# Kernel optimization log

Hardware: AMD Instinct MI355X
Metric: run time of the kernel (lower is better)

The kernel has to match this reference:

```python
import jax, jax.numpy as jnp
import numpy as np

D_MODEL = 2048
NUM_HEADS = 16
D_K = D_MODEL // NUM_HEADS


def setup_inputs() -> dict:
    key = jax.random.key(0)
    ks = jax.random.split(key, 12)
    B, S, D = 2, 2048, D_MODEL
    s = 1.0 / np.sqrt(D)
    return {
        "q": jax.random.normal(ks[0], (B, S, D), jnp.float32),
        "k": jax.random.normal(ks[1], (B, S, D), jnp.float32),
        "v": jax.random.normal(ks[2], (B, S, D), jnp.float32),
        "Wq": jax.random.normal(ks[3], (D, D), jnp.float32) * s,
        "bq": jax.random.normal(ks[4], (D,), jnp.float32) * 0.01,
        "Wk": jax.random.normal(ks[5], (D, D), jnp.float32) * s,
        "bk": jax.random.normal(ks[6], (D,), jnp.float32) * 0.01,
        "Wv": jax.random.normal(ks[7], (D, D), jnp.float32) * s,
        "bv": jax.random.normal(ks[8], (D,), jnp.float32) * 0.01,
        "Wo": jax.random.normal(ks[9], (D, D), jnp.float32) * s,
        "bo": jax.random.normal(ks[10], (D,), jnp.float32) * 0.01,
    }


def reference(q, k, v, Wq, bq, Wk, bk, Wv, bv, Wo, bo):
    B, S, D = q.shape
    H, dk = NUM_HEADS, D_K

    def proj(x, W, b):
        # Linear then split heads -> [B, H, S, dk]
        y = jnp.einsum('bsd,df->bsf', x, W) + b
        return y.reshape(B, -1, H, dk).transpose(0, 2, 1, 3)

    Q = proj(q, Wq, bq)
    K = proj(k, Wk, bk)
    V = proj(v, Wv, bv)

    scores = jnp.einsum('bhqd,bhkd->bhqk', Q, K) / jnp.sqrt(jnp.float32(dk))
    attn = jax.nn.softmax(scores, axis=-1)  # dropout is identity (eval)
    out = jnp.einsum('bhqk,bhkd->bhqd', attn, V)
    out = out.transpose(0, 2, 1, 3).reshape(B, -1, D)
    return jnp.einsum('bsd,df->bsf', out, Wo) + bo
```

## Files before the change

kernel.cpp:

```cpp
#include <hip/hip_runtime.h>
#include <hip/hip_bf16.h>
#include <stdint.h>

typedef float  f32x4  __attribute__((ext_vector_type(4)));
typedef float  f32x16 __attribute__((ext_vector_type(16)));
typedef short  s16x8  __attribute__((ext_vector_type(8)));

#define D_MODEL 2048
#define NHEADS  16
#define DK      128
#define BATCH   2
#define SEQ     2048
#define MROWS   (BATCH*SEQ)

__device__ __forceinline__ unsigned short f2bf(float f) {
  union { float f; unsigned int u; } v; v.f = f;
  unsigned int r = v.u + 0x7FFFu + ((v.u >> 16) & 1u);
  return (unsigned short)(r >> 16);
}

__device__ __forceinline__ unsigned int packbf_c(float lo, float hi) {
  __hip_bfloat16 l = __float2bfloat16(lo);
  __hip_bfloat16 h = __float2bfloat16(hi);
  unsigned short lu, hu;
  __builtin_memcpy(&lu, &l, 2);
  __builtin_memcpy(&hu, &h, 2);
  return (unsigned int)lu | ((unsigned int)hu << 16);
}

__device__ __forceinline__ void async16(const void* g, void* l) {
  __builtin_amdgcn_global_load_lds(
      (const __attribute__((address_space(1))) unsigned int*)g,
      (__attribute__((address_space(3))) unsigned int*)l,
      16, 0, 0);
}

__global__ __launch_bounds__(256) void f2b3_kernel(const float* __restrict__ q,
                                                   const float* __restrict__ k,
                                                   const float* __restrict__ v,
                                                   unsigned short* __restrict__ qb,
                                                   unsigned short* __restrict__ kb,
                                                   unsigned short* __restrict__ vb) {
  const float* s; unsigned short* d;
  switch (blockIdx.y) {
    case 0:  s = q; d = qb; break;
    case 1:  s = k; d = kb; break;
    default: s = v; d = vb; break;
  }
  int i = blockIdx.x * 256 + threadIdx.x;
  const float4* s4 = (const float4*)s;
  float4 a = s4[2*i];
  float4 b = s4[2*i+1];
  s16x8 o;
  o[0] = (short)f2bf(a.x); o[1] = (short)f2bf(a.y);
  o[2] = (short)f2bf(a.z); o[3] = (short)f2bf(a.w);
  o[4] = (short)f2bf(b.x); o[5] = (short)f2bf(b.y);
  o[6] = (short)f2bf(b.z); o[7] = (short)f2bf(b.w);
  *(s16x8*)(d + 8*(size_t)i) = o;
}

__global__ __launch_bounds__(256) void wtrans_kernel(const float* __restrict__ Wq,
                                                     const float* __restrict__ Wk,
                                                     const float* __restrict__ Wv,
                                                     const float* __restrict__ Wo,
                                                     unsigned short* __restrict__ WqT,
                                                     unsigned short* __restrict__ WkT,
                                                     unsigned short* __restrict__ WvT,
                                                     unsigned short* __restrict__ WoT) {
  const float* W; unsigned short* Wt;
  switch (blockIdx.z) {
    case 0:  W = Wq; Wt = WqT; break;
    case 1:  W = Wk; Wt = WkT; break;
    case 2:  W = Wv; Wt = WvT; break;
    default: W = Wo; Wt = WoT; break;
  }
  __shared__ float tl[32][33];
  int x = threadIdx.x, y = threadIdx.y;
  int n0 = blockIdx.x * 32, k0 = blockIdx.y * 32;
  #pragma unroll
  for (int j = 0; j < 32; j += 8)
    tl[y + j][x] = W[(size_t)(k0 + y + j) * D_MODEL + n0 + x];
  __syncthreads();
  #pragma unroll
  for (int j = 0; j < 32; j += 8)
    Wt[(size_t)(n0 + y + j) * D_MODEL + k0 + x] = f2bf(tl[x][y + j]);
}

__device__ __forceinline__ void gemm3b_core(const unsigned short* __restrict__ A,
                                            const unsigned short* __restrict__ Bt,
                                            const float* __restrict__ bias,
                                            void* __restrict__ Cout,
                                            int N, int K, int mode, float scale,
                                            int m0, int n0, char* lds) {
  const int t  = threadIdx.x;
  const int l  = t & 63, w = t >> 6;
  const int wm = w >> 1, wn = w & 1;
  const int lr = l & 15, lg = l >> 4;

  auto STAGE = [&](int slot, int kt) {
    char* Ad = lds + slot*49152;
    char* Bd = lds + slot*49152 + 32768;
    #pragma unroll
    for (int i = 0; i < 4; ++i) {
      int c = t + 512*i;
      int row = c >> 3, crs = (c & 7) ^ (row & 7);
      async16(A + (size_t)(m0 + row)*K + kt*64 + crs*8, Ad + c*16);
    }
    #pragma unroll
    for (int i = 0; i < 2; ++i) {
      int c = t + 512*i;
      int row = c >> 3, crs = (c & 7) ^ (row & 7);
      async16(Bt + (size_t)(n0 + row)*K + kt*64 + crs*8, Bd + c*16);
    }
  };

  const int NT = K >> 6;
  STAGE(0, 0);
  STAGE(1, 1);
  asm volatile("s_waitcnt vmcnt(6)" ::: "memory");
  __builtin_amdgcn_s_barrier();

  f32x4 acc[4][4] = {};

  for (int kt = 0; kt < NT; ++kt) {
    if (kt + 2 < NT) STAGE((kt + 2) % 3, kt + 2);
    const char* Ac = lds + (kt % 3)*49152;
    const char* Bc = lds + (kt % 3)*49152 + 32768;

    #pragma unroll
    for (int ks = 0; ks < 2; ++ks) {
      const int cb = ks*64 + lg*16;
      s16x8 af[4], bf[4];
      #pragma unroll
      for (int mf = 0; mf < 4; ++mf) {
        int row = wm*64 + mf*16 + lr;
        af[mf] = *(const s16x8*)(Ac + row*128 + (cb ^ ((row & 7) << 4)));
      }
      #pragma unroll
      for (int nf = 0; nf < 4; ++nf) {
        int row = wn*64 + nf*16 + lr;
        bf[nf] = *(const s16x8*)(Bc + row*128 + (cb ^ ((row & 7) << 4)));
      }
      __builtin_amdgcn_s_setprio(1);
      #pragma unroll
      for (int mf = 0; mf < 4; ++mf)
        #pragma unroll
        for (int nf = 0; nf < 4; ++nf)
          acc[mf][nf] = __builtin_amdgcn_mfma_f32_16x16x32_bf16(af[mf], bf[nf], acc[mf][nf], 0, 0, 0);
      __builtin_amdgcn_s_setprio(0);
    }

    if (kt + 1 < NT) {
      if (kt + 2 < NT) asm volatile("s_waitcnt vmcnt(6)" ::: "memory");
      else             asm volatile("s_waitcnt vmcnt(0)" ::: "memory");
      __builtin_amdgcn_s_barrier();
    }
  }

  if (mode == 0) {
    float* C = (float*)Cout;
    #pragma unroll
    for (int nf = 0; nf < 4; ++nf) {
      int col = n0 + wn*64 + nf*16 + lr;
      float bv = bias[col];
      #pragma unroll
      for (int mf = 0; mf < 4; ++mf) {
        int rowb = m0 + wm*64 + mf*16 + lg*4;
        #pragma unroll
        for (int r = 0; r < 4; ++r)
          C[(size_t)(rowb + r)*N + col] = (acc[mf][nf][r] + bv) * scale;
      }
    }
  } else {
    unsigned short* C = (unsigned short*)Cout;
    #pragma unroll
    for (int nf = 0; nf < 4; ++nf) {
      int col = n0 + wn*64 + nf*16 + lr;
      float bv = bias[col];
      int h = col >> 7, dkk = col & 127;
      #pragma unroll
      for (int mf = 0; mf < 4; ++mf) {
        int rowb = m0 + wm*64 + mf*16 + lg*4;
        #pragma unroll
        for (int r = 0; r < 4; ++r) {
          int row = rowb + r;
          int b = row >> 11, s = row & 2047;
          C[((size_t)((b*NHEADS + h)*SEQ + s))*DK + dkk] = f2bf((acc[mf][nf][r] + bv) * scale);
        }
      }
    }
  }
}

__device__ __forceinline__ void swz_mn(int& m0, int& n0) {
  int lin = blockIdx.y * 16 + blockIdx.x;
  int xcd = lin & 7;
  int pos = lin >> 3;
  n0 = (xcd*2 + (pos & 1)) * 128;
  m0 = (pos >> 1) * 256;
}

__global__ __launch_bounds__(512) void gemm256_qkv(const unsigned short* __restrict__ qb,
                                                   const unsigned short* __restrict__ kb,
                                                   const unsigned short* __restrict__ vb,
                                                   const unsigned short* __restrict__ WT,
                                                   const float* __restrict__ bq,
                                                   const float* __restrict__ bk,
                                                   const float* __restrict__ bv,
                                                   unsigned short* __restrict__ Hout,
                                                   float qscale) {
  __shared__ char lds[147456];
  const int z = blockIdx.z;
  const unsigned short* A = (z == 0) ? qb : (z == 1) ? kb : vb;
  const float* bias       = (z == 0) ? bq : (z == 1) ? bk : bv;
  const float scale       = (z == 0) ? qscale : 1.0f;
  const unsigned short* Bt = WT + (size_t)z * D_MODEL * D_MODEL;
  unsigned short* Cout     = Hout + (size_t)z * MROWS * D_MODEL;
  int m0, n0; swz_mn(m0, n0);
  gemm3b_core(A, Bt, bias, Cout, D_MODEL, D_MODEL, 1, scale, m0, n0, lds);
}

__global__ __launch_bounds__(512) void gemm256_out(const unsigned short* __restrict__ A,
                                                   const unsigned short* __restrict__ Bt,
                                                   const float* __restrict__ bias,
                                                   float* __restrict__ Cout) {
  __shared__ char lds[147456];
  int m0, n0; swz_mn(m0, n0);
  gemm3b_core(A, Bt, bias, Cout, D_MODEL, D_MODEL, 0, 1.0f, m0, n0, lds);
}

__global__ __launch_bounds__(256, 2) void attn_kernel(const unsigned short* __restrict__ Q,
                                                      const unsigned short* __restrict__ K,
                                                      const unsigned short* __restrict__ V,
                                                      unsigned short* __restrict__ O) {
  __shared__ char lds[64*256 + 128*144];
  unsigned short* Kl = (unsigned short*)lds;
  unsigned short* Vt = (unsigned short*)(lds + 64*256);

  const int t  = threadIdx.x;
  const int l  = t & 63, w = t >> 6;
  const int q_ = l & 31, hi = l >> 5;
  const int bh = blockIdx.y;
  const int b  = bh >> 4, h = bh & 15;
  const int q0 = blockIdx.x * 128;

  const unsigned short* Qp = Q + (size_t)bh * SEQ * DK;
  const unsigned short* Kp = K + (size_t)bh * SEQ * DK;
  const unsigned short* Vp = V + (size_t)bh * SEQ * DK;

  const int qrow = q0 + w*32 + q_;
  s16x8 aq[8];
  #pragma unroll
  for (int kk = 0; kk < 8; ++kk)
    aq[kk] = *(const s16x8*)(Qp + (size_t)qrow*DK + kk*16 + hi*8);

  f32x16 accO[4] = {};
  float m = -INFINITY, L = 0.f;

  const int vp_ = t & 31;
  const int vd0 = (t >> 5) * 8;

  const int NT = SEQ/64;
  s16x8 va0, vb0, va1, vb1;

  va0 = *(const s16x8*)(Vp + (size_t)(2*vp_    )*DK + vd0);
  vb0 = *(const s16x8*)(Vp + (size_t)(2*vp_ + 1)*DK + vd0);
  va1 = *(const s16x8*)(Vp + (size_t)(2*vp_    )*DK + vd0 + 64);
  vb1 = *(const s16x8*)(Vp + (size_t)(2*vp_ + 1)*DK + vd0 + 64);
  #pragma unroll
  for (int i = 0; i < 4; ++i) {
    int c   = t + 256*i;
    int row = c >> 4;
    int sb  = ((c & 15) << 4) ^ ((row & 15) << 4);
    async16((const char*)(Kp + (size_t)row*DK) + sb, (char*)Kl + c*16);
  }
  asm volatile("" ::: "memory");

  for (int tt = 0; tt < NT; ++tt) {
    asm volatile("s_waitcnt vmcnt(4)" ::: "memory");
    #pragma unroll
    for (int j = 0; j < 8; ++j) {
      unsigned int pk0 = (unsigned int)(unsigned short)va0[j]
                       | ((unsigned int)(unsigned short)vb0[j] << 16);
      *(unsigned int*)&Vt[(vd0 + j)*72 + 2*vp_] = pk0;
      unsigned int pk1 = (unsigned int)(unsigned short)va1[j]
                       | ((unsigned int)(unsigned short)vb1[j] << 16);
      *(unsigned int*)&Vt[(vd0 + 64 + j)*72 + 2*vp_] = pk1;
    }
    __syncthreads();

    f32x16 S0 = {}, S1 = {};
    __builtin_amdgcn_s_setprio(1);
    #pragma unroll
    for (int t2 = 0; t2 < 2; ++t2) {
      int krow = t2*32 + q_;
      const char* kb = (const char*)Kl + krow*256;
      int swz = (krow & 15) << 4;
      #pragma unroll
      for (int kk = 0; kk < 8; ++kk) {
        s16x8 kf = *(const s16x8*)(kb + ((kk*32 + hi*16) ^ swz));
        if (t2 == 0) S0 = __builtin_amdgcn_mfma_f32_32x32x16_bf16(kf, aq[kk], S0, 0, 0, 0);
        else         S1 = __builtin_amdgcn_mfma_f32_32x32x16_bf16(kf, aq[kk], S1, 0, 0, 0);
      }
    }
    __builtin_amdgcn_s_setprio(0);
    __syncthreads();

    if (tt + 1 < NT) {
      int kvn = (tt + 1) * 64;
      va0 = *(const s16x8*)(Vp + (size_t)(kvn + 2*vp_    )*DK + vd0);
      vb0 = *(const s16x8*)(Vp + (size_t)(kvn + 2*vp_ + 1)*DK + vd0);
      va1 = *(const s16x8*)(Vp + (size_t)(kvn + 2*vp_    )*DK + vd0 + 64);
      vb1 = *(const s16x8*)(Vp + (size_t)(kvn + 2*vp_ + 1)*DK + vd0 + 64);
      #pragma unroll
      for (int i = 0; i < 4; ++i) {
        int c   = t + 256*i;
        int row = c >> 4;
        int sb  = ((c & 15) << 4) ^ ((row & 15) << 4);
        async16((const char*)(Kp + (size_t)(kvn + row)*DK) + sb, (char*)Kl + c*16);
      }
      asm volatile("" ::: "memory");
    }

    f32x16 mx;
    #pragma unroll
    for (int r = 0; r < 16; ++r) mx[r] = fmaxf(S0[r], S1[r]);
    float m8_[8];
    #pragma unroll
    for (int r = 0; r < 8; ++r) m8_[r] = fmaxf(mx[r], mx[r+8]);
    float m4a = fmaxf(m8_[0], m8_[4]), m4b = fmaxf(m8_[1], m8_[5]);
    float m4c = fmaxf(m8_[2], m8_[6]), m4d = fmaxf(m8_[3], m8_[7]);
    float pmax = fmaxf(fmaxf(m4a, m4b), fmaxf(m4c, m4d));
    pmax = fmaxf(pmax, __shfl_xor(pmax, 32, 64));

    if (!__all(pmax <= m + 11.0f)) {
      float mnew = fmaxf(m, pmax);
      float corr = exp2f(m - mnew);
      m = mnew;
      L *= corr;
      #pragma unroll
      for (int sub = 0; sub < 4; ++sub)
        #pragma unroll
        for (int r = 0; r < 16; ++r) accO[sub][r] *= corr;
    }

    float rs0 = 0.f, rs1 = 0.f, rs2 = 0.f, rs3 = 0.f;
    #pragma unroll
    for (int r = 0; r < 4; ++r) {
      float a0 = exp2f(S0[r]    - m); S0[r]    = a0; rs0 += a0;
      float a1 = exp2f(S0[r+4]  - m); S0[r+4]  = a1; rs1 += a1;
      float a2 = exp2f(S0[r+8]  - m); S0[r+8]  = a2; rs2 += a2;
      float a3 = exp2f(S0[r+12] - m); S0[r+12] = a3; rs3 += a3;
      float b0 = exp2f(S1[r]    - m); S1[r]    = b0; rs0 += b0;
      float b1 = exp2f(S1[r+4]  - m); S1[r+4]  = b1; rs1 += b1;
      float b2 = exp2f(S1[r+8]  - m); S1[r+8]  = b2; rs2 += b2;
      float b3 = exp2f(S1[r+12] - m); S1[r+12] = b3; rs3 += b3;
    }
    float rs = (rs0 + rs1) + (rs2 + rs3);
    rs += __shfl_xor(rs, 32, 64);
    L += rs;

    s16x8 PB[4];
    #pragma unroll
    for (int t2 = 0; t2 < 2; ++t2) {
      #pragma unroll
      for (int half = 0; half < 2; ++half) {
        int bse = half*8;
        unsigned int pkA01, pkA23, pkB01, pkB23;
        if (t2 == 0) {
          pkA01 = packbf_c(S0[bse+0], S0[bse+1]);
          pkA23 = packbf_c(S0[bse+2], S0[bse+3]);
          pkB01 = packbf_c(S0[bse+4], S0[bse+5]);
          pkB23 = packbf_c(S0[bse+6], S0[bse+7]);
        } else {
          pkA01 = packbf_c(S1[bse+0], S1[bse+1]);
          pkA23 = packbf_c(S1[bse+2], S1[bse+3]);
          pkB01 = packbf_c(S1[bse+4], S1[bse+5]);
          pkB23 = packbf_c(S1[bse+6], S1[bse+7]);
        }
        unsigned int xA01 = __shfl_xor(pkA01, 32, 64);
        unsigned int xA23 = __shfl_xor(pkA23, 32, 64);
        unsigned int xB01 = __shfl_xor(pkB01, 32, 64);
        unsigned int xB23 = __shfl_xor(pkB23, 32, 64);
        union { unsigned int u[4]; s16x8 v; } f;
        f.u[0] = hi ? xB01 : pkA01;
        f.u[1] = hi ? xB23 : pkA23;
        f.u[2] = hi ? pkB01 : xA01;
        f.u[3] = hi ? pkB23 : xA23;
        PB[t2*2 + half] = f.v;
      }
    }

    __builtin_amdgcn_s_setprio(1);
    #pragma unroll
    for (int sub = 0; sub < 4; ++sub) {
      const char* vb2 = (const char*)Vt + (size_t)(sub*32 + q_)*144 + hi*16;
      #pragma unroll
      for (int kk = 0; kk < 4; ++kk) {
        s16x8 vf = *(const s16x8*)(vb2 + kk*32);
        accO[sub] = __builtin_amdgcn_mfma_f32_32x32x16_bf16(vf, PB[kk], accO[sub], 0, 0, 0);
      }
    }
    __builtin_amdgcn_s_setprio(0);

    __builtin_amdgcn_s_barrier();
  }

  __syncthreads();
  unsigned short* Ob = (unsigned short*)lds + (size_t)w*4096;
  float inv = 1.0f / L;
  #pragma unroll
  for (int sub = 0; sub < 4; ++sub)
    #pragma unroll
    for (int j = 0; j < 8; ++j) {
      unsigned int pw = packbf_c(accO[sub][2*j]*inv, accO[sub][2*j+1]*inv);
      int dv = sub*32 + (j&1)*2 + ((j>>1)*8) + 4*hi;
      *(unsigned int*)((char*)Ob + q_*256 + ((dv*2) ^ ((q_ & 15) << 4))) = pw;
    }
  asm volatile("s_waitcnt lgkmcnt(0)" ::: "memory");
  size_t gbase = ((size_t)(b*SEQ + q0 + w*32 + q_))*D_MODEL + h*DK;
  #pragma unroll
  for (int p = 0; p < 8; ++p) {
    int chunk = hi + 2*p;
    s16x8 ov = *(const s16x8*)((char*)Ob + q_*256 + ((chunk*16) ^ ((q_ & 15) << 4)));
    *(s16x8*)(O + gbase + chunk*8) = ov;
  }
}

extern "C" void kernel_launch(void* const* d_in, const int* in_sizes, int n_in,
                              void* d_out, int out_size, void* d_ws, size_t ws_size,
                              hipStream_t stream) {
  const float* q  = (const float*)d_in[0];
  const float* k  = (const float*)d_in[1];
  const float* v  = (const float*)d_in[2];
  const float* Wq = (const float*)d_in[3];
  const float* bq = (const float*)d_in[4];
  const float* Wk = (const float*)d_in[5];
  const float* bk = (const float*)d_in[6];
  const float* Wv = (const float*)d_in[7];
  const float* bv = (const float*)d_in[8];
  const float* Wo = (const float*)d_in[9];
  const float* bo = (const float*)d_in[10];
  float* out = (float*)d_out;

  char* ws = (char*)d_ws;
  const size_t SZT = (size_t)MROWS * D_MODEL * 2;
  const size_t SZW = (size_t)D_MODEL * D_MODEL * 2;

  unsigned short* qb  = (unsigned short*)(ws);
  unsigned short* kb  = (unsigned short*)(ws + SZT);
  unsigned short* vb  = (unsigned short*)(ws + 2*SZT);
  unsigned short* WqT = (unsigned short*)(ws + 3*SZT);
  unsigned short* WkT = (unsigned short*)(ws + 3*SZT + SZW);
  unsigned short* WvT = (unsigned short*)(ws + 3*SZT + 2*SZW);
  unsigned short* WoT = (unsigned short*)(ws + 3*SZT + 3*SZW);
  unsigned short* Qh  = (unsigned short*)(ws + 3*SZT + 4*SZW);
  unsigned short* Kh  = (unsigned short*)(ws + 4*SZT + 4*SZW);
  unsigned short* Vh  = (unsigned short*)(ws + 5*SZT + 4*SZW);
  unsigned short* Oc  = qb;

  const int n8 = MROWS * D_MODEL / 8;
  f2b3_kernel<<<dim3(n8/256, 3), 256, 0, stream>>>(q, k, v, qb, kb, vb);
  wtrans_kernel<<<dim3(64, 64, 4), dim3(32, 8), 0, stream>>>(Wq, Wk, Wv, Wo, WqT, WkT, WvT, WoT);

  const float qscale = 0.1275174308f;
  gemm256_qkv<<<dim3(16, 16, 3), 512, 0, stream>>>(qb, kb, vb, WqT, bq, bk, bv, Qh, qscale);

  attn_kernel<<<dim3(SEQ/128, BATCH*NHEADS), 256, 0, stream>>>(Qh, Kh, Vh, Oc);

  gemm256_out<<<dim3(16, 16), 512, 0, stream>>>(Oc, WoT, bo, out);
}
```

Measured before the change: 309.2 us.

## Emit V transposed from QKV GEMM and async-stage it into double-buffered LDS

The QKV projection GEMM gets a third epilogue mode that writes V in a [b,h,dk,seq] layout. The attention kernel can then stream V tiles straight into LDS with async copies, using an XOR swizzle and two buffers. This removes the per-tile register load, pack and transpose of V into LDS, and the trailing barrier at the end of each iteration. In exchange, the V GEMM epilogue now writes with a large stride and poorer coalescing. Correctness also relies on the loop-top __syncthreads waiting for the async V and K copies, since the explicit vmcnt wait was removed.

```diff
diff --git a/kernel.cpp b/kernel.cpp
--- a/kernel.cpp
+++ b/kernel.cpp
@@ -171,7 +171,7 @@
           C[(size_t)(rowb + r)*N + col] = (acc[mf][nf][r] + bv) * scale;
       }
     }
-  } else {
+  } else if (mode == 1) {
     unsigned short* C = (unsigned short*)Cout;
     #pragma unroll
     for (int nf = 0; nf < 4; ++nf) {
@@ -186,6 +186,24 @@
           int row = rowb + r;
           int b = row >> 11, s = row & 2047;
           C[((size_t)((b*NHEADS + h)*SEQ + s))*DK + dkk] = f2bf((acc[mf][nf][r] + bv) * scale);
+        }
+      }
+    }
+  } else {
+    unsigned short* C = (unsigned short*)Cout;
+    #pragma unroll
+    for (int nf = 0; nf < 4; ++nf) {
+      int col = n0 + wn*64 + nf*16 + lr;
+      float bv = bias[col];
+      int h = col >> 7, dkk = col & 127;
+      #pragma unroll
+      for (int mf = 0; mf < 4; ++mf) {
+        int rowb = m0 + wm*64 + mf*16 + lg*4;
+        #pragma unroll
+        for (int r = 0; r < 4; ++r) {
+          int row = rowb + r;
+          int b = row >> 11, s = row & 2047;
+          C[((size_t)((b*NHEADS + h)*DK + dkk))*SEQ + s] = f2bf((acc[mf][nf][r] + bv) * scale);
         }
       }
     }
@@ -214,10 +232,11 @@
   const unsigned short* A = (z == 0) ? qb : (z == 1) ? kb : vb;
   const float* bias       = (z == 0) ? bq : (z == 1) ? bk : bv;
   const float scale       = (z == 0) ? qscale : 1.0f;
+  const int   mode        = (z == 2) ? 2 : 1;
   const unsigned short* Bt = WT + (size_t)z * D_MODEL * D_MODEL;
   unsigned short* Cout     = Hout + (size_t)z * MROWS * D_MODEL;
   int m0, n0; swz_mn(m0, n0);
-  gemm3b_core(A, Bt, bias, Cout, D_MODEL, D_MODEL, 1, scale, m0, n0, lds);
+  gemm3b_core(A, Bt, bias, Cout, D_MODEL, D_MODEL, mode, scale, m0, n0, lds);
 }
 
 __global__ __launch_bounds__(512) void gemm256_out(const unsigned short* __restrict__ A,
@@ -231,11 +250,10 @@
 
 __global__ __launch_bounds__(256, 2) void attn_kernel(const unsigned short* __restrict__ Q,
                                                       const unsigned short* __restrict__ K,
-                                                      const unsigned short* __restrict__ V,
+                                                      const unsigned short* __restrict__ Vt_g,
                                                       unsigned short* __restrict__ O) {
-  __shared__ char lds[64*256 + 128*144];
+  __shared__ char lds[64*256 + 2*16384];
   unsigned short* Kl = (unsigned short*)lds;
-  unsigned short* Vt = (unsigned short*)(lds + 64*256);
 
   const int t  = threadIdx.x;
   const int l  = t & 63, w = t >> 6;
@@ -244,9 +262,9 @@
   const int b  = bh >> 4, h = bh & 15;
   const int q0 = blockIdx.x * 128;
 
-  const unsigned short* Qp = Q + (size_t)bh * SEQ * DK;
-  const unsigned short* Kp = K + (size_t)bh * SEQ * DK;
-  const unsigned short* Vp = V + (size_t)bh * SEQ * DK;
+  const unsigned short* Qp = Q    + (size_t)bh * SEQ * DK;
+  const unsigned short* Kp = K    + (size_t)bh * SEQ * DK;
+  const unsigned short* Vp = Vt_g + (size_t)bh * DK * SEQ;
 
   const int qrow = q0 + w*32 + q_;
   s16x8 aq[8];
@@ -257,36 +275,33 @@
   f32x16 accO[4] = {};
   float m = -INFINITY, L = 0.f;
 
-  const int vp_ = t & 31;
-  const int vd0 = (t >> 5) * 8;
-
   const int NT = SEQ/64;
-  s16x8 va0, vb0, va1, vb1;
-
-  va0 = *(const s16x8*)(Vp + (size_t)(2*vp_    )*DK + vd0);
-  vb0 = *(const s16x8*)(Vp + (size_t)(2*vp_ + 1)*DK + vd0);
-  va1 = *(const s16x8*)(Vp + (size_t)(2*vp_    )*DK + vd0 + 64);
-  vb1 = *(const s16x8*)(Vp + (size_t)(2*vp_ + 1)*DK + vd0 + 64);
-  #pragma unroll
-  for (int i = 0; i < 4; ++i) {
-    int c   = t + 256*i;
-    int row = c >> 4;
-    int sb  = ((c & 15) << 4) ^ ((row & 15) << 4);
-    async16((const char*)(Kp + (size_t)row*DK) + sb, (char*)Kl + c*16);
-  }
+
+  auto stageK = [&](int kv0) {
+    #pragma unroll
+    for (int i = 0; i < 4; ++i) {
+      int c   = t + 256*i;
+      int row = c >> 4;
+      int sb  = ((c & 15) << 4) ^ ((row & 15) << 4);
+      async16((const char*)(Kp + (size_t)(kv0 + row)*DK) + sb, (char*)Kl + c*16);
+    }
+  };
+  auto stageV = [&](int kv0, int buf) {
+    char* Vd = lds + 16384 + buf*16384;
+    #pragma unroll
+    for (int i = 0; i < 4; ++i) {
+      int c   = t + 256*i;
+      int row = c >> 3;
+      int sb  = ((c & 7) << 4) ^ ((row & 7) << 4);
+      async16((const char*)(Vp + (size_t)row*SEQ + kv0) + sb, Vd + c*16);
+    }
+  };
+
+  stageK(0);
+  stageV(0, 0);
   asm volatile("" ::: "memory");
 
   for (int tt = 0; tt < NT; ++tt) {
-    asm volatile("s_waitcnt vmcnt(4)" ::: "memory");
-    #pragma unroll
-    for (int j = 0; j < 8; ++j) {
-      unsigned int pk0 = (unsigned int)(unsigned short)va0[j]
-                       | ((unsigned int)(unsigned short)vb0[j] << 16);
-      *(unsigned int*)&Vt[(vd0 + j)*72 + 2*vp_] = pk0;
-      unsigned int pk1 = (unsigned int)(unsigned short)va1[j]
-                       | ((unsigned int)(unsigned short)vb1[j] << 16);
-      *(unsigned int*)&Vt[(vd0 + 64 + j)*72 + 2*vp_] = pk1;
-    }
     __syncthreads();
 
     f32x16 S0 = {}, S1 = {};
@@ -307,18 +322,8 @@
     __syncthreads();
 
     if (tt + 1 < NT) {
-      int kvn = (tt + 1) * 64;
-      va0 = *(const s16x8*)(Vp + (size_t)(kvn + 2*vp_    )*DK + vd0);
-      vb0 = *(const s16x8*)(Vp + (size_t)(kvn + 2*vp_ + 1)*DK + vd0);
-      va1 = *(const s16x8*)(Vp + (size_t)(kvn + 2*vp_    )*DK + vd0 + 64);
-      vb1 = *(const s16x8*)(Vp + (size_t)(kvn + 2*vp_ + 1)*DK + vd0 + 64);
-      #pragma unroll
-      for (int i = 0; i < 4; ++i) {
-        int c   = t + 256*i;
-        int row = c >> 4;
-        int sb  = ((c & 15) << 4) ^ ((row & 15) << 4);
-        async16((const char*)(Kp + (size_t)(kvn + row)*DK) + sb, (char*)Kl + c*16);
-      }
+      stageK((tt + 1) * 64);
+      stageV((tt + 1) * 64, (tt + 1) & 1);
       asm volatile("" ::: "memory");
     }
 
@@ -391,19 +396,20 @@
       }
     }
 
+    const char* Vc = lds + 16384 + (tt & 1)*16384;
     __builtin_amdgcn_s_setprio(1);
     #pragma unroll
     for (int sub = 0; sub < 4; ++sub) {
-      const char* vb2 = (const char*)Vt + (size_t)(sub*32 + q_)*144 + hi*16;
+      int row = sub*32 + q_;
+      const char* vb2 = Vc + row*128;
+      int swz = (row & 7) << 4;
       #pragma unroll
       for (int kk = 0; kk < 4; ++kk) {
-        s16x8 vf = *(const s16x8*)(vb2 + kk*32);
+        s16x8 vf = *(const s16x8*)(vb2 + ((kk*32 + hi*16) ^ swz));
         accO[sub] = __builtin_amdgcn_mfma_f32_32x32x16_bf16(vf, PB[kk], accO[sub], 0, 0, 0);
       }
     }
     __builtin_amdgcn_s_setprio(0);
-
-    __builtin_amdgcn_s_barrier();
   }
 
   __syncthreads();
```

Result: no change. 306.2 us (-1.0%).
